# Performance work log

Measured on AMD Instinct MI355X. Metric: run time of the kernel, lower is better.

## Reference

```python
import jax, jax.numpy as jnp
import numpy as np

N_TP = 4  # number of heterogeneous agent types (experts)


def _mlp(x, w1, b1, w2, b2, w3, b3):
    h = jax.nn.relu(x @ w1 + b1)
    h = jax.nn.relu(h @ w2 + b2)
    return h @ w3 + b3


def setup_inputs() -> dict:
    key = jax.random.key(0)
    ks = jax.random.split(key, 12)
    T, A, D, H, NA = 2048, 128, 64, 64, 16
    s = 0.05
    return {
        "obs": jax.random.normal(ks[0], (T, A, D), dtype=jnp.float32),
        "hete_pick": jax.random.randint(ks[1], (T, A), 0, N_TP, dtype=jnp.int64),
        "gp_sel_summary": jax.random.uniform(ks[2], (T, N_TP), dtype=jnp.float32),
        "W1": jax.random.normal(ks[3], (N_TP, D + N_TP, H), dtype=jnp.float32) * s,
        "b1": jnp.zeros((N_TP, H), jnp.float32),
        "W2": jax.random.normal(ks[4], (N_TP, H, H), dtype=jnp.float32) * s,
        "b2": jnp.zeros((N_TP, H), jnp.float32),
        "W3": jax.random.normal(ks[5], (N_TP, H, NA), dtype=jnp.float32) * s,
        "b3": jnp.zeros((N_TP, NA), jnp.float32),
        "cW1": jax.random.normal(ks[6], (D + N_TP, H), dtype=jnp.float32) * s,
        "cb1": jnp.zeros((H,), jnp.float32),
        "cW2": jax.random.normal(ks[7], (H, H), dtype=jnp.float32) * s,
        "cb2": jnp.zeros((H,), jnp.float32),
        "cW3": jax.random.normal(ks[8], (H, 1), dtype=jnp.float32) * s,
        "cb3": jnp.zeros((1,), jnp.float32),
    }


def reference(obs, hete_pick, gp_sel_summary, W1, b1, W2, b2, W3, b3,
              cW1, cb1, cW2, cb2, cW3, cb3):
    T, A, D = obs.shape
    n_tp = W1.shape[0]
    # hete_info_obs: broadcast group-selection summary over agents, concat to obs
    hete_info = jnp.broadcast_to(gp_sel_summary[:, None, :], (T, A, n_tp))
    x = jnp.concatenate([obs, hete_info.astype(obs.dtype)], axis=-1)  # [T,A,D+n_tp]
    xf = x.reshape(T * A, D + n_tp)
    tp = hete_pick.reshape(T * A)
    # per-type dispatch: mask -> sub-net -> scatter back (expressed as masked select)
    logits = jnp.zeros((T * A, W3.shape[-1]), obs.dtype)
    for t in range(n_tp):
        out_t = _mlp(xf, W1[t], b1[t], W2[t], b2[t], W3[t], b3[t])
        logits = jnp.where((tp == t)[:, None], out_t, logits)
    # central critic runs on all agents
    value = _mlp(xf, cW1, cb1, cW2, cb2, cW3, cb3)  # [T*A,1]
    out = jnp.concatenate([logits, value], axis=-1)  # [T*A, n_action+1]
    return out.reshape(T, A, -1)
```

## Files before the change

### kernel.cpp

```cpp
#include <hip/hip_runtime.h>
#include <stdint.h>


typedef float v4f __attribute__((ext_vector_type(4)));
typedef short v8s __attribute__((ext_vector_type(8)));
typedef short v4s __attribute__((ext_vector_type(4)));
typedef float v4fa __attribute__((ext_vector_type(4), aligned(4)));

#define XS_STR 72
#define HS_STR 136
#define WP2_OFF  30720
#define WP3_OFF  51200
#define WPB2_OFF 56320

#define SEL4(te, a0, a1, a2, a3) \
    ((te) < 2 ? ((te) == 0 ? (a0) : (a1)) : ((te) == 2 ? (a2) : (a3)))

static __device__ __forceinline__ short f2bf(float f) {
    union { __bf16 b; short s; } u;
    u.b = (__bf16)f;
    return u.s;
}

static __device__ __forceinline__ v4s pack4r(const v4f a) {
    v4s r;
    r[0] = f2bf(fmaxf(a[0], 0.f));
    r[1] = f2bf(fmaxf(a[1], 0.f));
    r[2] = f2bf(fmaxf(a[2], 0.f));
    r[3] = f2bf(fmaxf(a[3], 0.f));
    return r;
}

__global__ void prep_kernel(const float* __restrict__ W1, const float* __restrict__ cW1,
                            const float* __restrict__ W2, const float* __restrict__ cW2,
                            const float* __restrict__ W3, const float* __restrict__ cW3,
                            const float* __restrict__ b1, const float* __restrict__ cb1,
                            const float* __restrict__ b2, const float* __restrict__ cb2,
                            short* __restrict__ wp) {
    int b = blockIdx.x, lane = threadIdx.x;
    int nl = lane & 15, quad = lane >> 4;
    short frag[8];
    if (b < 60) {
        int e = b / 12, rem = b % 12, ks = rem / 4, nt = rem % 4;
        int n = nt * 16 + nl;
#pragma unroll
        for (int j = 0; j < 8; j++) {
            int k = ks * 32 + quad * 8 + j;
            float v = 0.f;
            if (k < 68)       v = (e < 4) ? W1[(e * 68 + k) * 64 + n] : cW1[k * 64 + n];
            else if (k == 68) v = (e < 4) ? b1[e * 64 + n] : cb1[n];
            frag[j] = f2bf(v);
        }
    } else if (b < 100) {
        int u = b - 60, e = u / 8, ks = (u % 8) / 4, nt = u % 4;
        int n = nt * 16 + nl;
#pragma unroll
        for (int j = 0; j < 8; j++) {
            int k = ks * 32 + quad * 8 + j;
            frag[j] = f2bf((e < 4) ? W2[(e * 64 + k) * 64 + n] : cW2[k * 64 + n]);
        }
    } else if (b < 110) {
        int u = b - 100;
#pragma unroll
        for (int j = 0; j < 8; j++) {
            int ks = (u < 8) ? (u & 1) : (u - 8);
            int k  = ks * 32 + quad * 8 + j;
            float v;
            if (u < 8) { int ee = u >> 1; v = W3[(ee * 64 + k) * 16 + nl]; }
            else       { v = (nl == 0) ? cW3[k] : 0.f; }
            frag[j] = f2bf(v);
        }
    } else {
        int u = b - 110, net = u / 4, nt = u % 4;
        int n = nt * 16 + nl;
#pragma unroll
        for (int j = 0; j < 8; j++) {
            float v = 0.f;
            if (quad == 0 && j == 0) v = (net < 4) ? b2[net * 64 + n] : cb2[n];
            frag[j] = f2bf(v);
        }
    }
    v8s pk = { frag[0], frag[1], frag[2], frag[3], frag[4], frag[5], frag[6], frag[7] };
    *(v8s*)(wp + (size_t)b * 512 + lane * 8) = pk;
}


__global__ __launch_bounds__(256, 4) void main_kernel(
    const float* __restrict__ obs, const int* __restrict__ hete,
    const float* __restrict__ gp, const short* __restrict__ wp,
    const float* __restrict__ b3, const float* __restrict__ cb3,
    float* __restrict__ out)
{
    __shared__ __align__(16) short buf[128 * HS_STR];
    __shared__ int rowtok[128];
    __shared__ int tslot[128];
    __shared__ int wcnt[2][4];

    short* xs = buf;
    short* hs = buf;

    const int b = blockIdx.x;
    const int tid = threadIdx.x, lane = tid & 63, w = tid >> 6;
    const int ml = lane & 15, quad = lane >> 4;
    const size_t base = (size_t)b * 128;

    const int ltk = tid >> 1, hh = tid & 1;
    const float4* src = (const float4*)(obs + (base + ltk) * 64 + hh * 32);
    float4 f[8];
#pragma unroll
    for (int t = 0; t < 8; t++) f[t] = src[t];

    const float* gpb = gp + (size_t)b * 4;
    float g0 = gpb[0], g1 = gpb[1], g2 = gpb[2], g3 = gpb[3];

    int e = 0, rank = 0;
    if (tid < 128) {
        e = hete[base + tid];
        unsigned long long ltm = (1ull << lane) - 1ull;
        unsigned long long m0 = __ballot(e == 0);
        unsigned long long m1 = __ballot(e == 1);
        unsigned long long m2 = __ballot(e == 2);
        unsigned long long m3 = __ballot(e == 3);
        if      (e == 0) rank = __popcll(m0 & ltm);
        else if (e == 1) rank = __popcll(m1 & ltm);
        else if (e == 2) rank = __popcll(m2 & ltm);
        else             rank = __popcll(m3 & ltm);
        if (lane == 0) {
            wcnt[w][0] = __popcll(m0); wcnt[w][1] = __popcll(m1);
            wcnt[w][2] = __popcll(m2); wcnt[w][3] = __popcll(m3);
        }
    }
    __syncthreads();

    const int c0 = wcnt[0][0] + wcnt[1][0];
    const int c1 = wcnt[0][1] + wcnt[1][1];
    const int c2 = wcnt[0][2] + wcnt[1][2];
    const int sgs1 = __builtin_amdgcn_readfirstlane(c0);
    const int sgs2 = __builtin_amdgcn_readfirstlane(c0 + c1);
    const int sgs3 = __builtin_amdgcn_readfirstlane(c0 + c1 + c2);
    const int SG[5] = { 0, sgs1, sgs2, sgs3, 128 };

    if (tid < 128) {
        int gsE  = SEL4(e, 0, sgs1, sgs2, sgs3);
        int woff = (w == 1) ? wcnt[0][e] : 0;
        int slot = gsE + woff + rank;
        rowtok[slot] = tid;
        tslot[tid]   = slot;
    }
    __syncthreads();

    {
        int s  = tslot[ltk];
        int rb = s * XS_STR + hh * 32;
#pragma unroll
        for (int t = 0; t < 4; t++) {
            float4 a0 = f[2 * t], a1 = f[2 * t + 1];
            v8s pk = { f2bf(a0.x), f2bf(a0.y), f2bf(a0.z), f2bf(a0.w),
                       f2bf(a1.x), f2bf(a1.y), f2bf(a1.z), f2bf(a1.w) };
            *(v8s*)&xs[rb + t * 8] = pk;
        }
    }

    v8s gfrag = (v8s){0,0,0,0,0,0,0,0};
    v8s onef  = (v8s){0,0,0,0,0,0,0,0};
    if (quad == 0) {
        gfrag[0] = f2bf(g0); gfrag[1] = f2bf(g1);
        gfrag[2] = f2bf(g2); gfrag[3] = f2bf(g3);
        gfrag[4] = (short)0x3F80;
        onef[0]  = (short)0x3F80;
    }
    __syncthreads();

    v4f accE[8], accC[8], fx[3];
#pragma unroll
    for (int mt = 0; mt < 8; mt++) { accE[mt] = (v4f){0,0,0,0}; }
    fx[0] = fx[1] = fx[2] = (v4f){0,0,0,0};

    {
        v8s cW2 = *(const v8s*)(wp + (size_t)(14 * 4 + w) * 512 + lane * 8);
        v4f tC = __builtin_amdgcn_mfma_f32_16x16x32_bf16(cW2, gfrag, (v4f){0,0,0,0}, 0, 0, 0);
#pragma unroll
        for (int mt = 0; mt < 8; mt++) accC[mt] = tC;
    }
#pragma unroll
    for (int te = 0; te < 4; te++) {
        int lo = SG[te], hi = SG[te + 1];
        if (lo < hi) {
            v8s aW2 = *(const v8s*)(wp + (size_t)((te * 3 + 2) * 4 + w) * 512 + lane * 8);
            v4f tE = __builtin_amdgcn_mfma_f32_16x16x32_bf16(aW2, gfrag, (v4f){0,0,0,0}, 0, 0, 0);
#pragma unroll
            for (int mt = 0; mt < 8; mt++)
                if (mt * 16 >= lo && mt * 16 < hi) accE[mt] = tE;
            if (te > 0 && (lo & 15)) fx[te - 1] = tE;
        }
    }

    v8s cf1[2];
#pragma unroll
    for (int ks = 0; ks < 2; ks++)
        cf1[ks] = *(const v8s*)(wp + (size_t)((12 + ks) * 4 + w) * 512 + lane * 8);

#pragma unroll
    for (int ks = 0; ks < 2; ks++) {
#pragma unroll
        for (int mt = 0; mt < 8; mt++) {
            v8s xb = *(const v8s*)&xs[(mt * 16 + ml) * XS_STR + ks * 32 + quad * 8];
            accC[mt] = __builtin_amdgcn_mfma_f32_16x16x32_bf16(cf1[ks], xb, accC[mt], 0, 0, 0);
        }
#pragma unroll
        for (int te = 0; te < 4; te++) {
            int lo = SG[te], hi = SG[te + 1];
            if (lo < hi) {
                v8s aW = *(const v8s*)(wp + (size_t)((te * 3 + ks) * 4 + w) * 512 + lane * 8);
#pragma unroll
                for (int mt = 0; mt < 8; mt++) {
                    if (mt * 16 >= lo && mt * 16 < hi) {
                        v8s xb = *(const v8s*)&xs[(mt * 16 + ml) * XS_STR + ks * 32 + quad * 8];
                        accE[mt] = __builtin_amdgcn_mfma_f32_16x16x32_bf16(aW, xb, accE[mt], 0, 0, 0);
                    }
                    if (te > 0 && (lo & 15) && (lo >> 4) == mt) {
                        v8s xb = *(const v8s*)&xs[(mt * 16 + ml) * XS_STR + ks * 32 + quad * 8];
                        fx[te - 1] = __builtin_amdgcn_mfma_f32_16x16x32_bf16(aW, xb, fx[te - 1], 0, 0, 0);
                    }
                }
            }
        }
    }
    __syncthreads();

    {
#pragma unroll
        for (int mt = 0; mt < 8; mt++) {
            int rb = (mt * 16 + ml) * HS_STR + w * 16 + quad * 4;
            *(v4s*)&hs[rb]      = pack4r(accE[mt]);
            *(v4s*)&hs[rb + 64] = pack4r(accC[mt]);
        }
#pragma unroll
        for (int bb = 0; bb < 3; bb++) {
            int lo = SG[bb + 1], hi = SG[bb + 2];
            if ((lo & 15) && lo < hi) {
                int row  = (lo >> 4) * 16 + ml;
                int erow = (row >= sgs1) + (row >= sgs2) + (row >= sgs3);
                if (erow == bb + 1)
                    *(v4s*)&hs[row * HS_STR + w * 16 + quad * 4] = pack4r(fx[bb]);
            }
        }
    }
    __syncthreads();

    v4f acc2E[8], acc2C[8], fx2[3];
#pragma unroll
    for (int mt = 0; mt < 8; mt++) { acc2E[mt] = (v4f){0,0,0,0}; }
    fx2[0] = fx2[1] = fx2[2] = (v4f){0,0,0,0};

    {
        v8s cbf = *(const v8s*)(wp + WPB2_OFF + (size_t)(16 + w) * 512 + lane * 8);
        v4f tC = __builtin_amdgcn_mfma_f32_16x16x32_bf16(cbf, onef, (v4f){0,0,0,0}, 0, 0, 0);
#pragma unroll
        for (int mt = 0; mt < 8; mt++) acc2C[mt] = tC;
    }
#pragma unroll
    for (int te = 0; te < 4; te++) {
        int lo = SG[te], hi = SG[te + 1];
        if (lo < hi) {
            v8s bf = *(const v8s*)(wp + WPB2_OFF + (size_t)(te * 4 + w) * 512 + lane * 8);
            v4f tE = __builtin_amdgcn_mfma_f32_16x16x32_bf16(bf, onef, (v4f){0,0,0,0}, 0, 0, 0);
#pragma unroll
            for (int mt = 0; mt < 8; mt++)
                if (mt * 16 >= lo && mt * 16 < hi) acc2E[mt] = tE;
            if (te > 0 && (lo & 15)) fx2[te - 1] = tE;
        }
    }

    v8s cf2[2];
#pragma unroll
    for (int ks = 0; ks < 2; ks++)
        cf2[ks] = *(const v8s*)(wp + WP2_OFF + (size_t)((8 + ks) * 4 + w) * 512 + lane * 8);

#pragma unroll
    for (int ks = 0; ks < 2; ks++) {
#pragma unroll
        for (int mt = 0; mt < 8; mt++) {
            v8s hC = *(const v8s*)&hs[(mt * 16 + ml) * HS_STR + 64 + ks * 32 + quad * 8];
            acc2C[mt] = __builtin_amdgcn_mfma_f32_16x16x32_bf16(cf2[ks], hC, acc2C[mt], 0, 0, 0);
        }
#pragma unroll
        for (int te = 0; te < 4; te++) {
            int lo = SG[te], hi = SG[te + 1];
            if (lo < hi) {
                v8s aW = *(const v8s*)(wp + WP2_OFF + (size_t)((te * 2 + ks) * 4 + w) * 512 + lane * 8);
#pragma unroll
                for (int mt = 0; mt < 8; mt++) {
                    if (mt * 16 >= lo && mt * 16 < hi) {
                        v8s hE = *(const v8s*)&hs[(mt * 16 + ml) * HS_STR + ks * 32 + quad * 8];
                        acc2E[mt] = __builtin_amdgcn_mfma_f32_16x16x32_bf16(aW, hE, acc2E[mt], 0, 0, 0);
                    }
                    if (te > 0 && (lo & 15) && (lo >> 4) == mt) {
                        v8s hE = *(const v8s*)&hs[(mt * 16 + ml) * HS_STR + ks * 32 + quad * 8];
                        fx2[te - 1] = __builtin_amdgcn_mfma_f32_16x16x32_bf16(aW, hE, fx2[te - 1], 0, 0, 0);
                    }
                }
            }
        }
    }
    __syncthreads();

    {
#pragma unroll
        for (int mt = 0; mt < 8; mt++) {
            int rb = (mt * 16 + ml) * HS_STR + w * 16 + quad * 4;
            *(v4s*)&hs[rb]      = pack4r(acc2E[mt]);
            *(v4s*)&hs[rb + 64] = pack4r(acc2C[mt]);
        }
#pragma unroll
        for (int bb = 0; bb < 3; bb++) {
            int lo = SG[bb + 1], hi = SG[bb + 2];
            if ((lo & 15) && lo < hi) {
                int row  = (lo >> 4) * 16 + ml;
                int erow = (row >= sgs1) + (row >= sgs2) + (row >= sgs3);
                if (erow == bb + 1)
                    *(v4s*)&hs[row * HS_STR + w * 16 + quad * 4] = pack4r(fx2[bb]);
            }
        }
    }
    __syncthreads();

    v4f accL[2], accV[2];
#pragma unroll
    for (int j = 0; j < 2; j++) { accL[j] = (v4f){0,0,0,0}; accV[j] = (v4f){0,0,0,0}; }

#pragma unroll
    for (int ks = 0; ks < 2; ks++) {
        v8s aV = *(const v8s*)(wp + WP3_OFF + (size_t)(8 + ks) * 512 + lane * 8);
#pragma unroll
        for (int j = 0; j < 2; j++) {
            int mt = w + 4 * j;
            int te = (mt * 16 >= sgs1) + (mt * 16 >= sgs2) + (mt * 16 >= sgs3);
            v8s aW = *(const v8s*)(wp + WP3_OFF + (size_t)(te * 2 + ks) * 512 + lane * 8);
            v8s hE = *(const v8s*)&hs[(mt * 16 + ml) * HS_STR + ks * 32 + quad * 8];
            v8s hC = *(const v8s*)&hs[(mt * 16 + ml) * HS_STR + 64 + ks * 32 + quad * 8];
            accL[j] = __builtin_amdgcn_mfma_f32_16x16x32_bf16(aW, hE, accL[j], 0, 0, 0);
            accV[j] = __builtin_amdgcn_mfma_f32_16x16x32_bf16(aV, hC, accV[j], 0, 0, 0);
        }
    }

    v4f fxL[3];
#pragma unroll
    for (int bb = 0; bb < 3; bb++) {
        fxL[bb] = (v4f){0,0,0,0};
        int lo = SG[bb + 1], hi = SG[bb + 2];
        int mtb = lo >> 4;
        if ((lo & 15) && lo < hi && (mtb & 3) == w) {
#pragma unroll
            for (int ks = 0; ks < 2; ks++) {
                v8s aW = *(const v8s*)(wp + WP3_OFF + (size_t)((bb + 1) * 2 + ks) * 512 + lane * 8);
                v8s hE = *(const v8s*)&hs[(mtb * 16 + ml) * HS_STR + ks * 32 + quad * 8];
                fxL[bb] = __builtin_amdgcn_mfma_f32_16x16x32_bf16(aW, hE, fxL[bb], 0, 0, 0);
            }
        }
    }

    {
        float cb3v = cb3[0];
#pragma unroll
        for (int j = 0; j < 2; j++) {
            int mt = w + 4 * j;
            int te = (mt * 16 >= sgs1) + (mt * 16 >= sgs2) + (mt * 16 >= sgs3);
            int row = mt * 16 + ml;
            int erow = (row >= sgs1) + (row >= sgs2) + (row >= sgs3);
            int tk = rowtok[row];
            float* o = out + (base + (size_t)tk) * 17;
            if (erow == te) {
                v4fa b3v = *(const v4fa*)(b3 + te * 16 + quad * 4);
                v4fa ov = { accL[j][0] + b3v[0], accL[j][1] + b3v[1],
                            accL[j][2] + b3v[2], accL[j][3] + b3v[3] };
                *(v4fa*)(o + quad * 4) = ov;
            }
            if (quad == 0) o[16] = accV[j][0] + cb3v;
        }
#pragma unroll
        for (int bb = 0; bb < 3; bb++) {
            int lo = SG[bb + 1], hi = SG[bb + 2];
            int mtb = lo >> 4;
            if ((lo & 15) && lo < hi && (mtb & 3) == w) {
                int row = mtb * 16 + ml;
                int erow = (row >= sgs1) + (row >= sgs2) + (row >= sgs3);
                if (erow == bb + 1) {
                    v4fa b3v = *(const v4fa*)(b3 + (bb + 1) * 16 + quad * 4);
                    int tk = rowtok[row];
                    float* o = out + (base + (size_t)tk) * 17;
                    v4fa ov = { fxL[bb][0] + b3v[0], fxL[bb][1] + b3v[1],
                                fxL[bb][2] + b3v[2], fxL[bb][3] + b3v[3] };
                    *(v4fa*)(o + quad * 4) = ov;
                }
            }
        }
    }
}


extern "C" void kernel_launch(void* const* d_in, const int* in_sizes, int n_in,
                              void* d_out, int out_size, void* d_ws, size_t ws_size,
                              hipStream_t stream) {
    const float* obs = (const float*)d_in[0];
    const int*  hete = (const int*)d_in[1];
    const float* gp  = (const float*)d_in[2];
    const float* W1  = (const float*)d_in[3];
    const float* b1  = (const float*)d_in[4];
    const float* W2  = (const float*)d_in[5];
    const float* b2  = (const float*)d_in[6];
    const float* W3  = (const float*)d_in[7];
    const float* b3  = (const float*)d_in[8];
    const float* cW1 = (const float*)d_in[9];
    const float* cb1 = (const float*)d_in[10];
    const float* cW2 = (const float*)d_in[11];
    const float* cb2 = (const float*)d_in[12];
    const float* cW3 = (const float*)d_in[13];
    const float* cb3 = (const float*)d_in[14];
    float* out = (float*)d_out;

    short* wp = (short*)d_ws;

    prep_kernel<<<130,  64, 0, stream>>>(W1, cW1, W2, cW2, W3, cW3,
                                         b1, cb1, b2, cb2, wp);
    main_kernel<<<2048, 256, 0, stream>>>(obs, hete, gp, wp, b3, cb3, out);
}
```

Baseline: 159.4 us.

## Give each wave whole row tiles across all three layers with per-wave LDS scratch

Reworks the work split so each wave owns two 16-row tiles end to end and computes all 64 hidden outputs for layers 1-3 itself. Intermediate activations go to a private per-wave LDS region, which removes the block-wide __syncthreads between layers. Rows are now gathered by token index instead of being scattered into sorted slots. In exchange, each wave loads all weight fragments for its tiles from global/L2 rather than sharing a quarter each. LDS use grows and register pressure may change.

```diff
diff --git a/kernel.cpp b/kernel.cpp
--- a/kernel.cpp
+++ b/kernel.cpp
@@ -8,13 +8,16 @@
 typedef float v4fa __attribute__((ext_vector_type(4), aligned(4)));
 
 #define XS_STR 72
-#define HS_STR 136
+#define SW_NET 1152
 #define WP2_OFF  30720
 #define WP3_OFF  51200
 #define WPB2_OFF 56320
 
 #define SEL4(te, a0, a1, a2, a3) \
     ((te) < 2 ? ((te) == 0 ? (a0) : (a1)) : ((te) == 2 ? (a2) : (a3)))
+
+#define MFMA __builtin_amdgcn_mfma_f32_16x16x32_bf16
+#define WFRAG(blk) (*(const v8s*)(wp + (size_t)(blk) * 512 + lane * 8))
 
 static __device__ __forceinline__ short f2bf(float f) {
     union { __bf16 b; short s; } u;
@@ -91,18 +94,16 @@
     const float* __restrict__ b3, const float* __restrict__ cb3,
     float* __restrict__ out)
 {
-    __shared__ __align__(16) short buf[128 * HS_STR];
+    __shared__ __align__(16) short buf[9216 + 4 * 2304];
     __shared__ int rowtok[128];
-    __shared__ int tslot[128];
     __shared__ int wcnt[2][4];
 
     short* xs = buf;
-    short* hs = buf;
-
-    const int b = blockIdx.x;
+
     const int tid = threadIdx.x, lane = tid & 63, w = tid >> 6;
     const int ml = lane & 15, quad = lane >> 4;
-    const size_t base = (size_t)b * 128;
+    const size_t base = (size_t)blockIdx.x * 128;
+    short* sw = buf + 9216 + w * 2304;
 
     const int ltk = tid >> 1, hh = tid & 1;
     const float4* src = (const float4*)(obs + (base + ltk) * 64 + hh * 32);
@@ -110,7 +111,7 @@
 #pragma unroll
     for (int t = 0; t < 8; t++) f[t] = src[t];
 
-    const float* gpb = gp + (size_t)b * 4;
+    const float* gpb = gp + (size_t)blockIdx.x * 4;
     float g0 = gpb[0], g1 = gpb[1], g2 = gpb[2], g3 = gpb[3];
 
     int e = 0, rank = 0;
@@ -138,20 +139,16 @@
     const int sgs1 = __builtin_amdgcn_readfirstlane(c0);
     const int sgs2 = __builtin_amdgcn_readfirstlane(c0 + c1);
     const int sgs3 = __builtin_amdgcn_readfirstlane(c0 + c1 + c2);
-    const int SG[5] = { 0, sgs1, sgs2, sgs3, 128 };
+    const int SGa[5] = { 0, sgs1, sgs2, sgs3, 128 };
 
     if (tid < 128) {
         int gsE  = SEL4(e, 0, sgs1, sgs2, sgs3);
         int woff = (w == 1) ? wcnt[0][e] : 0;
-        int slot = gsE + woff + rank;
-        rowtok[slot] = tid;
-        tslot[tid]   = slot;
-    }
-    __syncthreads();
+        rowtok[gsE + woff + rank] = tid;
+    }
 
     {
-        int s  = tslot[ltk];
-        int rb = s * XS_STR + hh * 32;
+        int rb = ltk * XS_STR + hh * 32;
 #pragma unroll
         for (int t = 0; t < 4; t++) {
             float4 a0 = f[2 * t], a1 = f[2 * t + 1];
@@ -160,6 +157,7 @@
             *(v8s*)&xs[rb + t * 8] = pk;
         }
     }
+    __syncthreads();
 
     v8s gfrag = (v8s){0,0,0,0,0,0,0,0};
     v8s onef  = (v8s){0,0,0,0,0,0,0,0};
@@ -169,231 +167,119 @@
         gfrag[4] = (short)0x3F80;
         onef[0]  = (short)0x3F80;
     }
-    __syncthreads();
-
-    v4f accE[8], accC[8], fx[3];
-#pragma unroll
-    for (int mt = 0; mt < 8; mt++) { accE[mt] = (v4f){0,0,0,0}; }
-    fx[0] = fx[1] = fx[2] = (v4f){0,0,0,0};
-
-    {
-        v8s cW2 = *(const v8s*)(wp + (size_t)(14 * 4 + w) * 512 + lane * 8);
-        v4f tC = __builtin_amdgcn_mfma_f32_16x16x32_bf16(cW2, gfrag, (v4f){0,0,0,0}, 0, 0, 0);
-#pragma unroll
-        for (int mt = 0; mt < 8; mt++) accC[mt] = tC;
-    }
-#pragma unroll
-    for (int te = 0; te < 4; te++) {
-        int lo = SG[te], hi = SG[te + 1];
-        if (lo < hi) {
-            v8s aW2 = *(const v8s*)(wp + (size_t)((te * 3 + 2) * 4 + w) * 512 + lane * 8);
-            v4f tE = __builtin_amdgcn_mfma_f32_16x16x32_bf16(aW2, gfrag, (v4f){0,0,0,0}, 0, 0, 0);
-#pragma unroll
-            for (int mt = 0; mt < 8; mt++)
-                if (mt * 16 >= lo && mt * 16 < hi) accE[mt] = tE;
-            if (te > 0 && (lo & 15)) fx[te - 1] = tE;
-        }
-    }
-
-    v8s cf1[2];
-#pragma unroll
-    for (int ks = 0; ks < 2; ks++)
-        cf1[ks] = *(const v8s*)(wp + (size_t)((12 + ks) * 4 + w) * 512 + lane * 8);
-
-#pragma unroll
-    for (int ks = 0; ks < 2; ks++) {
-#pragma unroll
-        for (int mt = 0; mt < 8; mt++) {
-            v8s xb = *(const v8s*)&xs[(mt * 16 + ml) * XS_STR + ks * 32 + quad * 8];
-            accC[mt] = __builtin_amdgcn_mfma_f32_16x16x32_bf16(cf1[ks], xb, accC[mt], 0, 0, 0);
-        }
-#pragma unroll
-        for (int te = 0; te < 4; te++) {
-            int lo = SG[te], hi = SG[te + 1];
-            if (lo < hi) {
-                v8s aW = *(const v8s*)(wp + (size_t)((te * 3 + ks) * 4 + w) * 512 + lane * 8);
-#pragma unroll
-                for (int mt = 0; mt < 8; mt++) {
-                    if (mt * 16 >= lo && mt * 16 < hi) {
-                        v8s xb = *(const v8s*)&xs[(mt * 16 + ml) * XS_STR + ks * 32 + quad * 8];
-                        accE[mt] = __builtin_amdgcn_mfma_f32_16x16x32_bf16(aW, xb, accE[mt], 0, 0, 0);
-                    }
-                    if (te > 0 && (lo & 15) && (lo >> 4) == mt) {
-                        v8s xb = *(const v8s*)&xs[(mt * 16 + ml) * XS_STR + ks * 32 + quad * 8];
-                        fx[te - 1] = __builtin_amdgcn_mfma_f32_16x16x32_bf16(aW, xb, fx[te - 1], 0, 0, 0);
-                    }
+    const float cb3v = cb3[0];
+
+#pragma unroll
+    for (int ntl = 0; ntl < 2; ++ntl) {
+        const int t   = 2 * w + ntl;
+        const int r0  = t * 16;
+        const int teT = (r0 >= sgs1) + (r0 >= sgs2) + (r0 >= sgs3);
+        const int pos = r0 + ml;
+        const int e_l = (pos >= sgs1) + (pos >= sgs2) + (pos >= sgs3);
+        const int tok = rowtok[pos];
+
+        v8s xb0 = *(const v8s*)&xs[tok * XS_STR + quad * 8];
+        v8s xb1 = *(const v8s*)&xs[tok * XS_STR + 32 + quad * 8];
+
+        v4f hE[4], aC[4];
+#pragma unroll
+        for (int m = 0; m < 4; m++) {
+            v4f v = MFMA(WFRAG((teT * 3 + 2) * 4 + m), gfrag, (v4f){0,0,0,0}, 0, 0, 0);
+            v = MFMA(WFRAG((teT * 3 + 0) * 4 + m), xb0, v, 0, 0, 0);
+            v = MFMA(WFRAG((teT * 3 + 1) * 4 + m), xb1, v, 0, 0, 0);
+            hE[m] = v;
+            v4f c = MFMA(WFRAG(14 * 4 + m), gfrag, (v4f){0,0,0,0}, 0, 0, 0);
+            c = MFMA(WFRAG(12 * 4 + m), xb0, c, 0, 0, 0);
+            c = MFMA(WFRAG(13 * 4 + m), xb1, c, 0, 0, 0);
+            aC[m] = c;
+        }
+#pragma unroll
+        for (int bb = 0; bb < 3; bb++) {
+            const int lo = SGa[bb + 1];
+            if ((lo & 15) && (lo >> 4) == t && lo < SGa[bb + 2]) {
+                const int te2 = bb + 1;
+#pragma unroll
+                for (int m = 0; m < 4; m++) {
+                    v4f v = MFMA(WFRAG((te2 * 3 + 2) * 4 + m), gfrag, (v4f){0,0,0,0}, 0, 0, 0);
+                    v = MFMA(WFRAG((te2 * 3 + 0) * 4 + m), xb0, v, 0, 0, 0);
+                    v = MFMA(WFRAG((te2 * 3 + 1) * 4 + m), xb1, v, 0, 0, 0);
+                    hE[m] = (e_l == te2) ? v : hE[m];
                 }
             }
         }
-    }
-    __syncthreads();
-
-    {
-#pragma unroll
-        for (int mt = 0; mt < 8; mt++) {
-            int rb = (mt * 16 + ml) * HS_STR + w * 16 + quad * 4;
-            *(v4s*)&hs[rb]      = pack4r(accE[mt]);
-            *(v4s*)&hs[rb + 64] = pack4r(accC[mt]);
+#pragma unroll
+        for (int m = 0; m < 4; m++) {
+            *(v4s*)&sw[ml * XS_STR + m * 16 + quad * 4]          = pack4r(hE[m]);
+            *(v4s*)&sw[SW_NET + ml * XS_STR + m * 16 + quad * 4] = pack4r(aC[m]);
+        }
+
+        v8s hbE0 = *(const v8s*)&sw[ml * XS_STR + quad * 8];
+        v8s hbE1 = *(const v8s*)&sw[ml * XS_STR + 32 + quad * 8];
+        v8s hbC0 = *(const v8s*)&sw[SW_NET + ml * XS_STR + quad * 8];
+        v8s hbC1 = *(const v8s*)&sw[SW_NET + ml * XS_STR + 32 + quad * 8];
+
+        v4f h2E[4], bC[4];
+#pragma unroll
+        for (int m = 0; m < 4; m++) {
+            v4f v = MFMA(WFRAG(WPB2_OFF / 512 + teT * 4 + m), onef, (v4f){0,0,0,0}, 0, 0, 0);
+            v = MFMA(WFRAG(WP2_OFF / 512 + (teT * 2 + 0) * 4 + m), hbE0, v, 0, 0, 0);
+            v = MFMA(WFRAG(WP2_OFF / 512 + (teT * 2 + 1) * 4 + m), hbE1, v, 0, 0, 0);
+            h2E[m] = v;
+            v4f c = MFMA(WFRAG(WPB2_OFF / 512 + 16 + m), onef, (v4f){0,0,0,0}, 0, 0, 0);
+            c = MFMA(WFRAG(WP2_OFF / 512 + (8 + 0) * 4 + m), hbC0, c, 0, 0, 0);
+            c = MFMA(WFRAG(WP2_OFF / 512 + (8 + 1) * 4 + m), hbC1, c, 0, 0, 0);
+            bC[m] = c;
         }
 #pragma unroll
         for (int bb = 0; bb < 3; bb++) {
-            int lo = SG[bb + 1], hi = SG[bb + 2];
-            if ((lo & 15) && lo < hi) {
-                int row  = (lo >> 4) * 16 + ml;
-                int erow = (row >= sgs1) + (row >= sgs2) + (row >= sgs3);
-                if (erow == bb + 1)
-                    *(v4s*)&hs[row * HS_STR + w * 16 + quad * 4] = pack4r(fx[bb]);
-            }
-        }
-    }
-    __syncthreads();
-
-    v4f acc2E[8], acc2C[8], fx2[3];
-#pragma unroll
-    for (int mt = 0; mt < 8; mt++) { acc2E[mt] = (v4f){0,0,0,0}; }
-    fx2[0] = fx2[1] = fx2[2] = (v4f){0,0,0,0};
-
-    {
-        v8s cbf = *(const v8s*)(wp + WPB2_OFF + (size_t)(16 + w) * 512 + lane * 8);
-        v4f tC = __builtin_amdgcn_mfma_f32_16x16x32_bf16(cbf, onef, (v4f){0,0,0,0}, 0, 0, 0);
-#pragma unroll
-        for (int mt = 0; mt < 8; mt++) acc2C[mt] = tC;
-    }
-#pragma unroll
-    for (int te = 0; te < 4; te++) {
-        int lo = SG[te], hi = SG[te + 1];
-        if (lo < hi) {
-            v8s bf = *(const v8s*)(wp + WPB2_OFF + (size_t)(te * 4 + w) * 512 + lane * 8);
-            v4f tE = __builtin_amdgcn_mfma_f32_16x16x32_bf16(bf, onef, (v4f){0,0,0,0}, 0, 0, 0);
-#pragma unroll
-            for (int mt = 0; mt < 8; mt++)
-                if (mt * 16 >= lo && mt * 16 < hi) acc2E[mt] = tE;
-            if (te > 0 && (lo & 15)) fx2[te - 1] = tE;
-        }
-    }
-
-    v8s cf2[2];
-#pragma unroll
-    for (int ks = 0; ks < 2; ks++)
-        cf2[ks] = *(const v8s*)(wp + WP2_OFF + (size_t)((8 + ks) * 4 + w) * 512 + lane * 8);
-
-#pragma unroll
-    for (int ks = 0; ks < 2; ks++) {
-#pragma unroll
-        for (int mt = 0; mt < 8; mt++) {
-            v8s hC = *(const v8s*)&hs[(mt * 16 + ml) * HS_STR + 64 + ks * 32 + quad * 8];
-            acc2C[mt] = __builtin_amdgcn_mfma_f32_16x16x32_bf16(cf2[ks], hC, acc2C[mt], 0, 0, 0);
-        }
-#pragma unroll
-        for (int te = 0; te < 4; te++) {
-            int lo = SG[te], hi = SG[te + 1];
-            if (lo < hi) {
-                v8s aW = *(const v8s*)(wp + WP2_OFF + (size_t)((te * 2 + ks) * 4 + w) * 512 + lane * 8);
-#pragma unroll
-                for (int mt = 0; mt < 8; mt++) {
-                    if (mt * 16 >= lo && mt * 16 < hi) {
-                        v8s hE = *(const v8s*)&hs[(mt * 16 + ml) * HS_STR + ks * 32 + quad * 8];
-                        acc2E[mt] = __builtin_amdgcn_mfma_f32_16x16x32_bf16(aW, hE, acc2E[mt], 0, 0, 0);
-                    }
-                    if (te > 0 && (lo & 15) && (lo >> 4) == mt) {
-                        v8s hE = *(const v8s*)&hs[(mt * 16 + ml) * HS_STR + ks * 32 + quad * 8];
-                        fx2[te - 1] = __builtin_amdgcn_mfma_f32_16x16x32_bf16(aW, hE, fx2[te - 1], 0, 0, 0);
-                    }
+            const int lo = SGa[bb + 1];
+            if ((lo & 15) && (lo >> 4) == t && lo < SGa[bb + 2]) {
+                const int te2 = bb + 1;
+#pragma unroll
+                for (int m = 0; m < 4; m++) {
+                    v4f v = MFMA(WFRAG(WPB2_OFF / 512 + te2 * 4 + m), onef, (v4f){0,0,0,0}, 0, 0, 0);
+                    v = MFMA(WFRAG(WP2_OFF / 512 + (te2 * 2 + 0) * 4 + m), hbE0, v, 0, 0, 0);
+                    v = MFMA(WFRAG(WP2_OFF / 512 + (te2 * 2 + 1) * 4 + m), hbE1, v, 0, 0, 0);
+                    h2E[m] = (e_l == te2) ? v : h2E[m];
                 }
             }
         }
-    }
-    __syncthreads();
-
-    {
-#pragma unroll
-        for (int mt = 0; mt < 8; mt++) {
-            int rb = (mt * 16 + ml) * HS_STR + w * 16 + quad * 4;
-            *(v4s*)&hs[rb]      = pack4r(acc2E[mt]);
-            *(v4s*)&hs[rb + 64] = pack4r(acc2C[mt]);
-        }
+#pragma unroll
+        for (int m = 0; m < 4; m++) {
+            *(v4s*)&sw[ml * XS_STR + m * 16 + quad * 4]          = pack4r(h2E[m]);
+            *(v4s*)&sw[SW_NET + ml * XS_STR + m * 16 + quad * 4] = pack4r(bC[m]);
+        }
+
+        v8s h2E0 = *(const v8s*)&sw[ml * XS_STR + quad * 8];
+        v8s h2E1 = *(const v8s*)&sw[ml * XS_STR + 32 + quad * 8];
+        v8s h2C0 = *(const v8s*)&sw[SW_NET + ml * XS_STR + quad * 8];
+        v8s h2C1 = *(const v8s*)&sw[SW_NET + ml * XS_STR + 32 + quad * 8];
+
+        v4f accL = MFMA(WFRAG(WP3_OFF / 512 + teT * 2 + 0), h2E0, (v4f){0,0,0,0}, 0, 0, 0);
+        accL     = MFMA(WFRAG(WP3_OFF / 512 + teT * 2 + 1), h2E1, accL, 0, 0, 0);
+        v4f accV = MFMA(WFRAG(WP3_OFF / 512 + 8), h2C0, (v4f){0,0,0,0}, 0, 0, 0);
+        accV     = MFMA(WFRAG(WP3_OFF / 512 + 9), h2C1, accV, 0, 0, 0);
+
 #pragma unroll
         for (int bb = 0; bb < 3; bb++) {
-            int lo = SG[bb + 1], hi = SG[bb + 2];
-            if ((lo & 15) && lo < hi) {
-                int row  = (lo >> 4) * 16 + ml;
-                int erow = (row >= sgs1) + (row >= sgs2) + (row >= sgs3);
-                if (erow == bb + 1)
-                    *(v4s*)&hs[row * HS_STR + w * 16 + quad * 4] = pack4r(fx2[bb]);
+            const int lo = SGa[bb + 1];
+            if ((lo & 15) && (lo >> 4) == t && lo < SGa[bb + 2]) {
+                const int te2 = bb + 1;
+                v4f v = MFMA(WFRAG(WP3_OFF / 512 + te2 * 2 + 0), h2E0, (v4f){0,0,0,0}, 0, 0, 0);
+                v     = MFMA(WFRAG(WP3_OFF / 512 + te2 * 2 + 1), h2E1, v, 0, 0, 0);
+#pragma unroll
+                for (int rr = 0; rr < 4; rr++)
+                    accL[rr] = (e_l == te2) ? v[rr] : accL[rr];
             }
         }
-    }
-    __syncthreads();
-
-    v4f accL[2], accV[2];
-#pragma unroll
-    for (int j = 0; j < 2; j++) { accL[j] = (v4f){0,0,0,0}; accV[j] = (v4f){0,0,0,0}; }
-
-#pragma unroll
-    for (int ks = 0; ks < 2; ks++) {
-        v8s aV = *(const v8s*)(wp + WP3_OFF + (size_t)(8 + ks) * 512 + lane * 8);
-#pragma unroll
-        for (int j = 0; j < 2; j++) {
-            int mt = w + 4 * j;
-            int te = (mt * 16 >= sgs1) + (mt * 16 >= sgs2) + (mt * 16 >= sgs3);
-            v8s aW = *(const v8s*)(wp + WP3_OFF + (size_t)(te * 2 + ks) * 512 + lane * 8);
-            v8s hE = *(const v8s*)&hs[(mt * 16 + ml) * HS_STR + ks * 32 + quad * 8];
-            v8s hC = *(const v8s*)&hs[(mt * 16 + ml) * HS_STR + 64 + ks * 32 + quad * 8];
-            accL[j] = __builtin_amdgcn_mfma_f32_16x16x32_bf16(aW, hE, accL[j], 0, 0, 0);
-            accV[j] = __builtin_amdgcn_mfma_f32_16x16x32_bf16(aV, hC, accV[j], 0, 0, 0);
-        }
-    }
-
-    v4f fxL[3];
-#pragma unroll
-    for (int bb = 0; bb < 3; bb++) {
-        fxL[bb] = (v4f){0,0,0,0};
-        int lo = SG[bb + 1], hi = SG[bb + 2];
-        int mtb = lo >> 4;
-        if ((lo & 15) && lo < hi && (mtb & 3) == w) {
-#pragma unroll
-            for (int ks = 0; ks < 2; ks++) {
-                v8s aW = *(const v8s*)(wp + WP3_OFF + (size_t)((bb + 1) * 2 + ks) * 512 + lane * 8);
-                v8s hE = *(const v8s*)&hs[(mtb * 16 + ml) * HS_STR + ks * 32 + quad * 8];
-                fxL[bb] = __builtin_amdgcn_mfma_f32_16x16x32_bf16(aW, hE, fxL[bb], 0, 0, 0);
-            }
-        }
-    }
-
-    {
-        float cb3v = cb3[0];
-#pragma unroll
-        for (int j = 0; j < 2; j++) {
-            int mt = w + 4 * j;
-            int te = (mt * 16 >= sgs1) + (mt * 16 >= sgs2) + (mt * 16 >= sgs3);
-            int row = mt * 16 + ml;
-            int erow = (row >= sgs1) + (row >= sgs2) + (row >= sgs3);
-            int tk = rowtok[row];
-            float* o = out + (base + (size_t)tk) * 17;
-            if (erow == te) {
-                v4fa b3v = *(const v4fa*)(b3 + te * 16 + quad * 4);
-                v4fa ov = { accL[j][0] + b3v[0], accL[j][1] + b3v[1],
-                            accL[j][2] + b3v[2], accL[j][3] + b3v[3] };
-                *(v4fa*)(o + quad * 4) = ov;
-            }
-            if (quad == 0) o[16] = accV[j][0] + cb3v;
-        }
-#pragma unroll
-        for (int bb = 0; bb < 3; bb++) {
-            int lo = SG[bb + 1], hi = SG[bb + 2];
-            int mtb = lo >> 4;
-            if ((lo & 15) && lo < hi && (mtb & 3) == w) {
-                int row = mtb * 16 + ml;
-                int erow = (row >= sgs1) + (row >= sgs2) + (row >= sgs3);
-                if (erow == bb + 1) {
-                    v4fa b3v = *(const v4fa*)(b3 + (bb + 1) * 16 + quad * 4);
-                    int tk = rowtok[row];
-                    float* o = out + (base + (size_t)tk) * 17;
-                    v4fa ov = { fxL[bb][0] + b3v[0], fxL[bb][1] + b3v[1],
-                                fxL[bb][2] + b3v[2], fxL[bb][3] + b3v[3] };
-                    *(v4fa*)(o + quad * 4) = ov;
-                }
-            }
+
+        {
+            const v4fa b3v = *(const v4fa*)(b3 + e_l * 16 + quad * 4);
+            float* o = out + (base + (size_t)tok) * 17;
+            v4fa ov = { accL[0] + b3v[0], accL[1] + b3v[1],
+                        accL[2] + b3v[2], accL[3] + b3v[3] };
+            *(v4fa*)(o + quad * 4) = ov;
+            if (quad == 0) o[16] = accV[0] + cb3v;
         }
     }
 }
```

Result: no change. 161.3 us (+1.2%).

## Double-buffer LDS, preload weight fragments into registers, gather rows via token indices

Applied to the files above, without the earlier changes.

Obs is now written to shared memory in token order and layer-1 reads gather rows through a per-row token index, which removes the tslot table and one barrier. Two LDS buffers alternate between layers so the barrier after each MFMA phase can go. All weight fragments for each layer are loaded into registers ahead of use to hide global latency. The last layer is restructured to compute the boundary-tile expert fix-ups inline and issue one store per row. Launch bounds drop to 2 blocks per SM so the larger register and LDS footprint fits, which lowers occupancy.

```diff
diff --git a/kernel.cpp b/kernel.cpp
--- a/kernel.cpp
+++ b/kernel.cpp
@@ -9,12 +9,15 @@
 
 #define XS_STR 72
 #define HS_STR 136
-#define WP2_OFF  30720
-#define WP3_OFF  51200
-#define WPB2_OFF 56320
+#define WP2B 60
+#define WP3B 100
+#define WPBB 110
 
 #define SEL4(te, a0, a1, a2, a3) \
     ((te) < 2 ? ((te) == 0 ? (a0) : (a1)) : ((te) == 2 ? (a2) : (a3)))
+
+#define MFMA __builtin_amdgcn_mfma_f32_16x16x32_bf16
+#define WFRAG(blk) (*(const v8s*)(wp + (size_t)(blk) * 512 + lane * 8))
 
 static __device__ __forceinline__ short f2bf(float f) {
     union { __bf16 b; short s; } u;
@@ -85,24 +88,24 @@
 }
 
 
-__global__ __launch_bounds__(256, 4) void main_kernel(
+__global__ __launch_bounds__(256, 2) void main_kernel(
     const float* __restrict__ obs, const int* __restrict__ hete,
     const float* __restrict__ gp, const short* __restrict__ wp,
     const float* __restrict__ b3, const float* __restrict__ cb3,
     float* __restrict__ out)
 {
-    __shared__ __align__(16) short buf[128 * HS_STR];
+    __shared__ __align__(16) short bufA[128 * HS_STR];
+    __shared__ __align__(16) short bufB[128 * HS_STR];
     __shared__ int rowtok[128];
-    __shared__ int tslot[128];
     __shared__ int wcnt[2][4];
 
-    short* xs = buf;
-    short* hs = buf;
-
-    const int b = blockIdx.x;
+    short* xs = bufA;
+    short* h1 = bufB;
+    short* h2 = bufA;
+
     const int tid = threadIdx.x, lane = tid & 63, w = tid >> 6;
     const int ml = lane & 15, quad = lane >> 4;
-    const size_t base = (size_t)b * 128;
+    const size_t base = (size_t)blockIdx.x * 128;
 
     const int ltk = tid >> 1, hh = tid & 1;
     const float4* src = (const float4*)(obs + (base + ltk) * 64 + hh * 32);
@@ -110,7 +113,16 @@
 #pragma unroll
     for (int t = 0; t < 8; t++) f[t] = src[t];
 
-    const float* gpb = gp + (size_t)b * 4;
+    v8s eW1[4][3], cW1f[3];
+#pragma unroll
+    for (int te = 0; te < 4; te++)
+#pragma unroll
+        for (int ks = 0; ks < 3; ks++)
+            eW1[te][ks] = WFRAG((te * 3 + ks) * 4 + w);
+#pragma unroll
+    for (int ks = 0; ks < 3; ks++) cW1f[ks] = WFRAG((12 + ks) * 4 + w);
+
+    const float* gpb = gp + (size_t)blockIdx.x * 4;
     float g0 = gpb[0], g1 = gpb[1], g2 = gpb[2], g3 = gpb[3];
 
     int e = 0, rank = 0;
@@ -143,15 +155,11 @@
     if (tid < 128) {
         int gsE  = SEL4(e, 0, sgs1, sgs2, sgs3);
         int woff = (w == 1) ? wcnt[0][e] : 0;
-        int slot = gsE + woff + rank;
-        rowtok[slot] = tid;
-        tslot[tid]   = slot;
-    }
-    __syncthreads();
+        rowtok[gsE + woff + rank] = tid;
+    }
 
     {
-        int s  = tslot[ltk];
-        int rb = s * XS_STR + hh * 32;
+        int rb = ltk * XS_STR + hh * 32;
 #pragma unroll
         for (int t = 0; t < 4; t++) {
             float4 a0 = f[2 * t], a1 = f[2 * t + 1];
@@ -160,6 +168,11 @@
             *(v8s*)&xs[rb + t * 8] = pk;
         }
     }
+    __syncthreads();
+
+    int tokR[8];
+#pragma unroll
+    for (int mt = 0; mt < 8; mt++) tokR[mt] = rowtok[mt * 16 + ml];
 
     v8s gfrag = (v8s){0,0,0,0,0,0,0,0};
     v8s onef  = (v8s){0,0,0,0,0,0,0,0};
@@ -169,16 +182,12 @@
         gfrag[4] = (short)0x3F80;
         onef[0]  = (short)0x3F80;
     }
-    __syncthreads();
 
     v4f accE[8], accC[8], fx[3];
-#pragma unroll
-    for (int mt = 0; mt < 8; mt++) { accE[mt] = (v4f){0,0,0,0}; }
     fx[0] = fx[1] = fx[2] = (v4f){0,0,0,0};
 
     {
-        v8s cW2 = *(const v8s*)(wp + (size_t)(14 * 4 + w) * 512 + lane * 8);
-        v4f tC = __builtin_amdgcn_mfma_f32_16x16x32_bf16(cW2, gfrag, (v4f){0,0,0,0}, 0, 0, 0);
+        v4f tC = MFMA(cW1f[2], gfrag, (v4f){0,0,0,0}, 0, 0, 0);
 #pragma unroll
         for (int mt = 0; mt < 8; mt++) accC[mt] = tC;
     }
@@ -186,8 +195,7 @@
     for (int te = 0; te < 4; te++) {
         int lo = SG[te], hi = SG[te + 1];
         if (lo < hi) {
-            v8s aW2 = *(const v8s*)(wp + (size_t)((te * 3 + 2) * 4 + w) * 512 + lane * 8);
-            v4f tE = __builtin_amdgcn_mfma_f32_16x16x32_bf16(aW2, gfrag, (v4f){0,0,0,0}, 0, 0, 0);
+            v4f tE = MFMA(eW1[te][2], gfrag, (v4f){0,0,0,0}, 0, 0, 0);
 #pragma unroll
             for (int mt = 0; mt < 8; mt++)
                 if (mt * 16 >= lo && mt * 16 < hi) accE[mt] = tE;
@@ -195,67 +203,67 @@
         }
     }
 
-    v8s cf1[2];
-#pragma unroll
-    for (int ks = 0; ks < 2; ks++)
-        cf1[ks] = *(const v8s*)(wp + (size_t)((12 + ks) * 4 + w) * 512 + lane * 8);
-
 #pragma unroll
     for (int ks = 0; ks < 2; ks++) {
-#pragma unroll
-        for (int mt = 0; mt < 8; mt++) {
-            v8s xb = *(const v8s*)&xs[(mt * 16 + ml) * XS_STR + ks * 32 + quad * 8];
-            accC[mt] = __builtin_amdgcn_mfma_f32_16x16x32_bf16(cf1[ks], xb, accC[mt], 0, 0, 0);
-        }
+        v8s xr[8];
+#pragma unroll
+        for (int mt = 0; mt < 8; mt++)
+            xr[mt] = *(const v8s*)&xs[tokR[mt] * XS_STR + ks * 32 + quad * 8];
+#pragma unroll
+        for (int mt = 0; mt < 8; mt++)
+            accC[mt] = MFMA(cW1f[ks], xr[mt], accC[mt], 0, 0, 0);
 #pragma unroll
         for (int te = 0; te < 4; te++) {
             int lo = SG[te], hi = SG[te + 1];
             if (lo < hi) {
-                v8s aW = *(const v8s*)(wp + (size_t)((te * 3 + ks) * 4 + w) * 512 + lane * 8);
 #pragma unroll
                 for (int mt = 0; mt < 8; mt++) {
-                    if (mt * 16 >= lo && mt * 16 < hi) {
-                        v8s xb = *(const v8s*)&xs[(mt * 16 + ml) * XS_STR + ks * 32 + quad * 8];
-                        accE[mt] = __builtin_amdgcn_mfma_f32_16x16x32_bf16(aW, xb, accE[mt], 0, 0, 0);
-                    }
-                    if (te > 0 && (lo & 15) && (lo >> 4) == mt) {
-                        v8s xb = *(const v8s*)&xs[(mt * 16 + ml) * XS_STR + ks * 32 + quad * 8];
-                        fx[te - 1] = __builtin_amdgcn_mfma_f32_16x16x32_bf16(aW, xb, fx[te - 1], 0, 0, 0);
-                    }
+                    if (mt * 16 >= lo && mt * 16 < hi)
+                        accE[mt] = MFMA(eW1[te][ks], xr[mt], accE[mt], 0, 0, 0);
+                    if (te > 0 && (lo & 15) && (lo >> 4) == mt)
+                        fx[te - 1] = MFMA(eW1[te][ks], xr[mt], fx[te - 1], 0, 0, 0);
                 }
             }
         }
     }
-    __syncthreads();
+
+    v8s eW2[4][2], cW2f[2], bE2[4], bC2;
+#pragma unroll
+    for (int te = 0; te < 4; te++) {
+#pragma unroll
+        for (int ks = 0; ks < 2; ks++)
+            eW2[te][ks] = WFRAG(WP2B + (te * 2 + ks) * 4 + w);
+        bE2[te] = WFRAG(WPBB + te * 4 + w);
+    }
+#pragma unroll
+    for (int ks = 0; ks < 2; ks++) cW2f[ks] = WFRAG(WP2B + (8 + ks) * 4 + w);
+    bC2 = WFRAG(WPBB + 16 + w);
 
     {
 #pragma unroll
         for (int mt = 0; mt < 8; mt++) {
             int rb = (mt * 16 + ml) * HS_STR + w * 16 + quad * 4;
-            *(v4s*)&hs[rb]      = pack4r(accE[mt]);
-            *(v4s*)&hs[rb + 64] = pack4r(accC[mt]);
+            *(v4s*)&h1[rb]      = pack4r(accE[mt]);
+            *(v4s*)&h1[rb + 64] = pack4r(accC[mt]);
         }
 #pragma unroll
         for (int bb = 0; bb < 3; bb++) {
-            int lo = SG[bb + 1], hi = SG[bb + 2];
-            if ((lo & 15) && lo < hi) {
+            int lo = SG[bb + 1];
+            if ((lo & 15) && lo < SG[bb + 2]) {
                 int row  = (lo >> 4) * 16 + ml;
-                int erow = (row >= sgs1) + (row >= sgs2) + (row >= sgs3);
-                if (erow == bb + 1)
-                    *(v4s*)&hs[row * HS_STR + w * 16 + quad * 4] = pack4r(fx[bb]);
+                int el   = (row >= sgs1) + (row >= sgs2) + (row >= sgs3);
+                if (el == bb + 1)
+                    *(v4s*)&h1[row * HS_STR + w * 16 + quad * 4] = pack4r(fx[bb]);
             }
         }
     }
     __syncthreads();
 
     v4f acc2E[8], acc2C[8], fx2[3];
-#pragma unroll
-    for (int mt = 0; mt < 8; mt++) { acc2E[mt] = (v4f){0,0,0,0}; }
     fx2[0] = fx2[1] = fx2[2] = (v4f){0,0,0,0};
 
     {
-        v8s cbf = *(const v8s*)(wp + WPB2_OFF + (size_t)(16 + w) * 512 + lane * 8);
-        v4f tC = __builtin_amdgcn_mfma_f32_16x16x32_bf16(cbf, onef, (v4f){0,0,0,0}, 0, 0, 0);
+        v4f tC = MFMA(bC2, onef, (v4f){0,0,0,0}, 0, 0, 0);
 #pragma unroll
         for (int mt = 0; mt < 8; mt++) acc2C[mt] = tC;
     }
@@ -263,8 +271,7 @@
     for (int te = 0; te < 4; te++) {
         int lo = SG[te], hi = SG[te + 1];
         if (lo < hi) {
-            v8s bf = *(const v8s*)(wp + WPB2_OFF + (size_t)(te * 4 + w) * 512 + lane * 8);
-            v4f tE = __builtin_amdgcn_mfma_f32_16x16x32_bf16(bf, onef, (v4f){0,0,0,0}, 0, 0, 0);
+            v4f tE = MFMA(bE2[te], onef, (v4f){0,0,0,0}, 0, 0, 0);
 #pragma unroll
             for (int mt = 0; mt < 8; mt++)
                 if (mt * 16 >= lo && mt * 16 < hi) acc2E[mt] = tE;
@@ -272,129 +279,97 @@
         }
     }
 
-    v8s cf2[2];
-#pragma unroll
-    for (int ks = 0; ks < 2; ks++)
-        cf2[ks] = *(const v8s*)(wp + WP2_OFF + (size_t)((8 + ks) * 4 + w) * 512 + lane * 8);
-
 #pragma unroll
     for (int ks = 0; ks < 2; ks++) {
+        v8s hrE[8], hrC[8];
 #pragma unroll
         for (int mt = 0; mt < 8; mt++) {
-            v8s hC = *(const v8s*)&hs[(mt * 16 + ml) * HS_STR + 64 + ks * 32 + quad * 8];
-            acc2C[mt] = __builtin_amdgcn_mfma_f32_16x16x32_bf16(cf2[ks], hC, acc2C[mt], 0, 0, 0);
-        }
+            int rb = (mt * 16 + ml) * HS_STR + ks * 32 + quad * 8;
+            hrE[mt] = *(const v8s*)&h1[rb];
+            hrC[mt] = *(const v8s*)&h1[rb + 64];
+        }
+#pragma unroll
+        for (int mt = 0; mt < 8; mt++)
+            acc2C[mt] = MFMA(cW2f[ks], hrC[mt], acc2C[mt], 0, 0, 0);
 #pragma unroll
         for (int te = 0; te < 4; te++) {
             int lo = SG[te], hi = SG[te + 1];
             if (lo < hi) {
-                v8s aW = *(const v8s*)(wp + WP2_OFF + (size_t)((te * 2 + ks) * 4 + w) * 512 + lane * 8);
 #pragma unroll
                 for (int mt = 0; mt < 8; mt++) {
-                    if (mt * 16 >= lo && mt * 16 < hi) {
-                        v8s hE = *(const v8s*)&hs[(mt * 16 + ml) * HS_STR + ks * 32 + quad * 8];
-                        acc2E[mt] = __builtin_amdgcn_mfma_f32_16x16x32_bf16(aW, hE, acc2E[mt], 0, 0, 0);
-                    }
-                    if (te > 0 && (lo & 15) && (lo >> 4) == mt) {
-                        v8s hE = *(const v8s*)&hs[(mt * 16 + ml) * HS_STR + ks * 32 + quad * 8];
-                        fx2[te - 1] = __builtin_amdgcn_mfma_f32_16x16x32_bf16(aW, hE, fx2[te - 1], 0, 0, 0);
-                    }
+                    if (mt * 16 >= lo && mt * 16 < hi)
+                        acc2E[mt] = MFMA(eW2[te][ks], hrE[mt], acc2E[mt], 0, 0, 0);
+                    if (te > 0 && (lo & 15) && (lo >> 4) == mt)
+                        fx2[te - 1] = MFMA(eW2[te][ks], hrE[mt], fx2[te - 1], 0, 0, 0);
                 }
             }
         }
     }
-    __syncthreads();
+
+    const int teA3 = ((w * 16) >= sgs1) + ((w * 16) >= sgs2) + ((w * 16) >= sgs3);
+    const int teB3 = (((w + 4) * 16) >= sgs1) + (((w + 4) * 16) >= sgs2) + (((w + 4) * 16) >= sgs3);
+    v8s wA0 = WFRAG(WP3B + teA3 * 2 + 0), wA1 = WFRAG(WP3B + teA3 * 2 + 1);
+    v8s wB0 = WFRAG(WP3B + teB3 * 2 + 0), wB1 = WFRAG(WP3B + teB3 * 2 + 1);
+    v8s wV0 = WFRAG(WP3B + 8), wV1 = WFRAG(WP3B + 9);
 
     {
 #pragma unroll
         for (int mt = 0; mt < 8; mt++) {
             int rb = (mt * 16 + ml) * HS_STR + w * 16 + quad * 4;
-            *(v4s*)&hs[rb]      = pack4r(acc2E[mt]);
-            *(v4s*)&hs[rb + 64] = pack4r(acc2C[mt]);
+            *(v4s*)&h2[rb]      = pack4r(acc2E[mt]);
+            *(v4s*)&h2[rb + 64] = pack4r(acc2C[mt]);
         }
 #pragma unroll
         for (int bb = 0; bb < 3; bb++) {
-            int lo = SG[bb + 1], hi = SG[bb + 2];
-            if ((lo & 15) && lo < hi) {
+            int lo = SG[bb + 1];
+            if ((lo & 15) && lo < SG[bb + 2]) {
                 int row  = (lo >> 4) * 16 + ml;
-                int erow = (row >= sgs1) + (row >= sgs2) + (row >= sgs3);
-                if (erow == bb + 1)
-                    *(v4s*)&hs[row * HS_STR + w * 16 + quad * 4] = pack4r(fx2[bb]);
+                int el   = (row >= sgs1) + (row >= sgs2) + (row >= sgs3);
+                if (el == bb + 1)
+                    *(v4s*)&h2[row * HS_STR + w * 16 + quad * 4] = pack4r(fx2[bb]);
             }
         }
     }
     __syncthreads();
 
-    v4f accL[2], accV[2];
-#pragma unroll
-    for (int j = 0; j < 2; j++) { accL[j] = (v4f){0,0,0,0}; accV[j] = (v4f){0,0,0,0}; }
-
-#pragma unroll
-    for (int ks = 0; ks < 2; ks++) {
-        v8s aV = *(const v8s*)(wp + WP3_OFF + (size_t)(8 + ks) * 512 + lane * 8);
-#pragma unroll
-        for (int j = 0; j < 2; j++) {
-            int mt = w + 4 * j;
-            int te = (mt * 16 >= sgs1) + (mt * 16 >= sgs2) + (mt * 16 >= sgs3);
-            v8s aW = *(const v8s*)(wp + WP3_OFF + (size_t)(te * 2 + ks) * 512 + lane * 8);
-            v8s hE = *(const v8s*)&hs[(mt * 16 + ml) * HS_STR + ks * 32 + quad * 8];
-            v8s hC = *(const v8s*)&hs[(mt * 16 + ml) * HS_STR + 64 + ks * 32 + quad * 8];
-            accL[j] = __builtin_amdgcn_mfma_f32_16x16x32_bf16(aW, hE, accL[j], 0, 0, 0);
-            accV[j] = __builtin_amdgcn_mfma_f32_16x16x32_bf16(aV, hC, accV[j], 0, 0, 0);
-        }
-    }
-
-    v4f fxL[3];
-#pragma unroll
-    for (int bb = 0; bb < 3; bb++) {
-        fxL[bb] = (v4f){0,0,0,0};
-        int lo = SG[bb + 1], hi = SG[bb + 2];
-        int mtb = lo >> 4;
-        if ((lo & 15) && lo < hi && (mtb & 3) == w) {
-#pragma unroll
-            for (int ks = 0; ks < 2; ks++) {
-                v8s aW = *(const v8s*)(wp + WP3_OFF + (size_t)((bb + 1) * 2 + ks) * 512 + lane * 8);
-                v8s hE = *(const v8s*)&hs[(mtb * 16 + ml) * HS_STR + ks * 32 + quad * 8];
-                fxL[bb] = __builtin_amdgcn_mfma_f32_16x16x32_bf16(aW, hE, fxL[bb], 0, 0, 0);
+    const float cb3v = cb3[0];
+#pragma unroll
+    for (int j = 0; j < 2; j++) {
+        const int mt  = w + 4 * j;
+        const int row = mt * 16 + ml;
+        const int el  = (row >= sgs1) + (row >= sgs2) + (row >= sgs3);
+        const int tok = tokR[mt];
+
+        int rb = row * HS_STR + quad * 8;
+        v8s hE0 = *(const v8s*)&h2[rb];
+        v8s hE1 = *(const v8s*)&h2[rb + 32];
+        v8s hC0 = *(const v8s*)&h2[rb + 64];
+        v8s hC1 = *(const v8s*)&h2[rb + 96];
+
+        v8s w0 = j ? wB0 : wA0, w1 = j ? wB1 : wA1;
+        v4f accL = MFMA(w0, hE0, (v4f){0,0,0,0}, 0, 0, 0);
+        accL     = MFMA(w1, hE1, accL, 0, 0, 0);
+        v4f accV = MFMA(wV0, hC0, (v4f){0,0,0,0}, 0, 0, 0);
+        accV     = MFMA(wV1, hC1, accV, 0, 0, 0);
+
+#pragma unroll
+        for (int bb = 0; bb < 3; bb++) {
+            int lo = SG[bb + 1];
+            if ((lo & 15) && lo < SG[bb + 2] && (lo >> 4) == mt) {
+                v4f v = MFMA(WFRAG(WP3B + (bb + 1) * 2 + 0), hE0, (v4f){0,0,0,0}, 0, 0, 0);
+                v     = MFMA(WFRAG(WP3B + (bb + 1) * 2 + 1), hE1, v, 0, 0, 0);
+#pragma unroll
+                for (int rr = 0; rr < 4; rr++)
+                    accL[rr] = (el == bb + 1) ? v[rr] : accL[rr];
             }
         }
-    }
-
-    {
-        float cb3v = cb3[0];
-#pragma unroll
-        for (int j = 0; j < 2; j++) {
-            int mt = w + 4 * j;
-            int te = (mt * 16 >= sgs1) + (mt * 16 >= sgs2) + (mt * 16 >= sgs3);
-            int row = mt * 16 + ml;
-            int erow = (row >= sgs1) + (row >= sgs2) + (row >= sgs3);
-            int tk = rowtok[row];
-            float* o = out + (base + (size_t)tk) * 17;
-            if (erow == te) {
-                v4fa b3v = *(const v4fa*)(b3 + te * 16 + quad * 4);
-                v4fa ov = { accL[j][0] + b3v[0], accL[j][1] + b3v[1],
-                            accL[j][2] + b3v[2], accL[j][3] + b3v[3] };
-                *(v4fa*)(o + quad * 4) = ov;
-            }
-            if (quad == 0) o[16] = accV[j][0] + cb3v;
-        }
-#pragma unroll
-        for (int bb = 0; bb < 3; bb++) {
-            int lo = SG[bb + 1], hi = SG[bb + 2];
-            int mtb = lo >> 4;
-            if ((lo & 15) && lo < hi && (mtb & 3) == w) {
-                int row = mtb * 16 + ml;
-                int erow = (row >= sgs1) + (row >= sgs2) + (row >= sgs3);
-                if (erow == bb + 1) {
-                    v4fa b3v = *(const v4fa*)(b3 + (bb + 1) * 16 + quad * 4);
-                    int tk = rowtok[row];
-                    float* o = out + (base + (size_t)tk) * 17;
-                    v4fa ov = { fxL[bb][0] + b3v[0], fxL[bb][1] + b3v[1],
-                                fxL[bb][2] + b3v[2], fxL[bb][3] + b3v[3] };
-                    *(v4fa*)(o + quad * 4) = ov;
-                }
-            }
-        }
+
+        const v4fa b3v = *(const v4fa*)(b3 + el * 16 + quad * 4);
+        float* o = out + (base + (size_t)tok) * 17;
+        v4fa ov = { accL[0] + b3v[0], accL[1] + b3v[1],
+                    accL[2] + b3v[2], accL[3] + b3v[3] };
+        *(v4fa*)(o + quad * 4) = ov;
+        if (quad == 0) o[16] = accV[0] + cb3v;
     }
 }
 
```

Measured after the change: 170.1 us. 6.7% more time.
